# Kernel tuning notes

Measured on AMD Instinct MI355X. Metric: run time of the kernel, lower is better.

The kernel has to match this reference:

```python
import jax, jax.numpy as jnp
import numpy as np

K = 4
REG_MAX = 32


def setup_inputs() -> dict:
    key = jax.random.key(0)
    ks = jax.random.split(key, 6)
    B, L, C = 8, 100000, 80
    scores = jax.random.normal(ks[0], (B, L, C), dtype=jnp.float32)
    pred_corners = jax.random.normal(ks[1], (B, L, 4 * (REG_MAX + 1)), dtype=jnp.float32)
    in_dim = 4 * (K + 1)  # 20
    hidden = 64
    w1 = jax.random.normal(ks[2], (in_dim, hidden), dtype=jnp.float32) * (1.0 / np.sqrt(in_dim))
    b1 = jax.random.normal(ks[3], (hidden,), dtype=jnp.float32) * 0.01
    w2 = jax.random.normal(ks[4], (hidden, 1), dtype=jnp.float32) * (1.0 / np.sqrt(hidden))
    b2 = jax.random.normal(ks[5], (1,), dtype=jnp.float32) * 0.01
    return {"scores": scores, "pred_corners": pred_corners,
            "w1": w1, "b1": b1, "w2": w2, "b2": b2}


def reference(scores, pred_corners, w1, b1, w2, b2):
    B, L, _ = pred_corners.shape
    # [B, L, 4, reg_max+1]
    prob = jax.nn.softmax(pred_corners.reshape(B, L, 4, REG_MAX + 1), axis=-1)
    topk, _ = jax.lax.top_k(prob, K)                       # [B, L, 4, k]
    stat = jnp.concatenate([topk, topk.mean(-1, keepdims=True)], axis=-1)  # [B, L, 4, k+1]
    stat = stat.reshape(B, L, 4 * (K + 1))                 # [B, L, 20]
    h = jax.nn.silu(stat @ w1 + b1)                        # [B, L, 64]
    quality = h @ w2 + b2                                  # [B, L, 1]
    return scores + quality
```

## Files before the change

### kernel.cpp

```cpp
#include <hip/hip_runtime.h>

#define LOG2E 1.4426950408889634f

typedef __attribute__((address_space(3))) unsigned int lds_u32_t;
typedef const __attribute__((address_space(1))) unsigned int glb_u32_t;

__global__ __launch_bounds__(256) void lqe_wave(
    const float* __restrict__ scores,
    const float* __restrict__ pred,
    const float* __restrict__ w1,
    const float* __restrict__ b1,
    const float* __restrict__ w2,
    const float* __restrict__ b2,
    float* __restrict__ out)
{
    __shared__ __align__(16) float predS[4 * 2112];
    __shared__ __align__(16) float wS[1412];

    const int t    = threadIdx.x;
    const int lane = t & 63;
    const int wv   = t >> 6;
    const int tile = blockIdx.x;

#pragma unroll
    for (int k = 0; k < 5; ++k) wS[t + 256 * k] = w1[t + 256 * k];
    if (t < 64) { wS[1280 + t] = b1[t]; wS[1344 + t] = w2[t]; }
    if (t == 0) wS[1408] = b2[0];
    __syncthreads();

    const float* gp  = pred + (size_t)tile * 8448 + wv * 2112;
    float*       buf = predS + wv * 2112;
#pragma unroll
    for (int k = 0; k < 8; ++k) {
        __builtin_amdgcn_global_load_lds((glb_u32_t*)(gp + 256 * k + 4 * lane),
                                         (lds_u32_t*)(buf + 256 * k), 16, 0, 0);
    }
    __builtin_amdgcn_global_load_lds((glb_u32_t*)(gp + 2048 + lane),
                                     (lds_u32_t*)(buf + 2048), 4, 0, 0);

    asm volatile("s_waitcnt vmcnt(0)" ::: "memory");
    __builtin_amdgcn_sched_barrier(0);

    const size_t s4 = (size_t)tile * 1280 + wv * 320;
    const float4* sp = reinterpret_cast<const float4*>(scores) + s4;
    float4 sv0 = sp[lane +   0];
    float4 sv1 = sp[lane +  64];
    float4 sv2 = sp[lane + 128];
    float4 sv3 = sp[lane + 192];
    float4 sv4 = sp[lane + 256];

    const int r = lane >> 2, c = lane & 3;
    const float* xp = buf + r * 132 + c * 33;
    float xs[33];
#pragma unroll
    for (int j = 0; j < 33; ++j) xs[j] = xp[j];

    float t0 = -1e30f, t1 = -1e30f, t2 = -1e30f, t3 = -1e30f;
#pragma unroll
    for (int j = 0; j < 33; ++j) {
        float v  = xs[j];
        float r0 = fminf(t0, v);  t0 = fmaxf(t0, v);
        float r1 = fminf(t1, r0); t1 = fmaxf(t1, r0);
        float r2 = fminf(t2, r1); t2 = fmaxf(t2, r1);
        t3 = fmaxf(t3, r2);
    }
    float denom = 0.f;
#pragma unroll
    for (int j = 0; j < 33; ++j)
        denom += __builtin_amdgcn_exp2f((xs[j] - t0) * LOG2E);
    float rd = __builtin_amdgcn_rcpf(denom);

    float s5[5];
    s5[0] = rd;
    s5[1] = __builtin_amdgcn_exp2f((t1 - t0) * LOG2E) * rd;
    s5[2] = __builtin_amdgcn_exp2f((t2 - t0) * LOG2E) * rd;
    s5[3] = __builtin_amdgcn_exp2f((t3 - t0) * LOG2E) * rd;
    s5[4] = (s5[0] + s5[1] + s5[2] + s5[3]) * 0.25f;

    float stat[20];
#pragma unroll
    for (int i = 0; i < 20; ++i)
        stat[i] = __shfl(s5[i % 5], i / 5, 4);

    float hacc[16];
    {
        const float4* b1v = reinterpret_cast<const float4*>(wS + 1280 + 16 * c);
#pragma unroll
        for (int k = 0; k < 4; ++k) {
            float4 b = b1v[k];
            hacc[4*k+0]=b.x; hacc[4*k+1]=b.y; hacc[4*k+2]=b.z; hacc[4*k+3]=b.w;
        }
    }
#pragma unroll
    for (int i = 0; i < 20; ++i) {
        const float si = stat[i];
        const float4* wv4 = reinterpret_cast<const float4*>(wS + i * 64 + 16 * c);
#pragma unroll
        for (int k = 0; k < 4; ++k) {
            float4 w = wv4[k];
            hacc[4*k+0] = fmaf(si, w.x, hacc[4*k+0]);
            hacc[4*k+1] = fmaf(si, w.y, hacc[4*k+1]);
            hacc[4*k+2] = fmaf(si, w.z, hacc[4*k+2]);
            hacc[4*k+3] = fmaf(si, w.w, hacc[4*k+3]);
        }
    }
    float q = 0.f;
    {
        const float4* w2v = reinterpret_cast<const float4*>(wS + 1344 + 16 * c);
#pragma unroll
        for (int k = 0; k < 4; ++k) {
            float4 w = w2v[k];
#pragma unroll
            for (int e = 0; e < 4; ++e) {
                float v  = hacc[4*k+e];
                float sg = __builtin_amdgcn_rcpf(1.f + __builtin_amdgcn_exp2f(-v * LOG2E));
                float we = (e == 0) ? w.x : (e == 1) ? w.y : (e == 2) ? w.z : w.w;
                q = fmaf(v * sg, we, q);
            }
        }
    }
    q += __shfl_xor(q, 1, 4);
    q += __shfl_xor(q, 2, 4);
    q += wS[1408];

    float4* op = reinterpret_cast<float4*>(out) + s4;
    {
        float qq; int idx, rl;
        idx = lane +   0; rl = idx / 20; qq = __shfl(q, rl * 4, 64);
        sv0.x+=qq; sv0.y+=qq; sv0.z+=qq; sv0.w+=qq; op[idx] = sv0;
        idx = lane +  64; rl = idx / 20; qq = __shfl(q, rl * 4, 64);
        sv1.x+=qq; sv1.y+=qq; sv1.z+=qq; sv1.w+=qq; op[idx] = sv1;
        idx = lane + 128; rl = idx / 20; qq = __shfl(q, rl * 4, 64);
        sv2.x+=qq; sv2.y+=qq; sv2.z+=qq; sv2.w+=qq; op[idx] = sv2;
        idx = lane + 192; rl = idx / 20; qq = __shfl(q, rl * 4, 64);
        sv3.x+=qq; sv3.y+=qq; sv3.z+=qq; sv3.w+=qq; op[idx] = sv3;
        idx = lane + 256; rl = idx / 20; qq = __shfl(q, rl * 4, 64);
        sv4.x+=qq; sv4.y+=qq; sv4.z+=qq; sv4.w+=qq; op[idx] = sv4;
    }
}

extern "C" void kernel_launch(void* const* d_in, const int* in_sizes, int n_in,
                              void* d_out, int out_size, void* d_ws, size_t ws_size,
                              hipStream_t stream) {
    const float* scores = (const float*)d_in[0];
    const float* pred   = (const float*)d_in[1];
    const float* w1     = (const float*)d_in[2];
    const float* b1     = (const float*)d_in[3];
    const float* w2     = (const float*)d_in[4];
    const float* b2     = (const float*)d_in[5];
    float* out = (float*)d_out;

    const int nrows = in_sizes[1] / 132;
    const int grid  = nrows / 64;

    hipLaunchKernelGGL(lqe_wave, dim3(grid), dim3(256), 0, stream,
                       scores, pred, w1, b1, w2, b2, out);
}
```

Measured before the change: 172.5 us.

## Compute MLP hidden layer with fp16 MFMA and overlap weight staging with loads

Replaces the per-lane scalar FMA loop for the 20x64 first layer with one 16x16x32 f16 MFMA per 16-column block. Stat rows go through LDS and weights are packed to fp16. Weight staging now happens after the async global-to-LDS prefetch is issued, so the loads overlap it, and the second-layer reduction uses xor shuffles plus an LDS broadcast of q. This cuts VALU work and register pressure (launch bounds now request 4 blocks), but it adds fp16 rounding of the inputs and weights and extra LDS round trips.

```diff
diff --git a/kernel.cpp b/kernel.cpp
--- a/kernel.cpp
+++ b/kernel.cpp
@@ -4,8 +4,14 @@
 
 typedef __attribute__((address_space(3))) unsigned int lds_u32_t;
 typedef const __attribute__((address_space(1))) unsigned int glb_u32_t;
+typedef __fp16 h2v __attribute__((ext_vector_type(2)));
+typedef __fp16 v8h __attribute__((ext_vector_type(8)));
+typedef float  v4f __attribute__((ext_vector_type(4)));
 
-__global__ __launch_bounds__(256) void lqe_wave(
+union H2U { h2v h; unsigned int u; };
+union V8U { unsigned int u[4]; v8h v; };
+
+__global__ __launch_bounds__(256, 4) void lqe_mfma(
     const float* __restrict__ scores,
     const float* __restrict__ pred,
     const float* __restrict__ w1,
@@ -15,45 +21,50 @@
     float* __restrict__ out)
 {
     __shared__ __align__(16) float predS[4 * 2112];
-    __shared__ __align__(16) float wS[1412];
+    __shared__ __align__(16) unsigned int wHf[1024];
+    __shared__ __align__(16) float wSf[129];
+    __shared__ __align__(16) float qS[4][16];
 
-    const int t    = threadIdx.x;
-    const int lane = t & 63;
-    const int wv   = t >> 6;
+    const int t = threadIdx.x, lane = t & 63, wv = t >> 6;
     const int tile = blockIdx.x;
+    float* buf = predS + wv * 2112;
 
+    const float* gp = pred + (size_t)tile * 8448 + wv * 2112;
 #pragma unroll
-    for (int k = 0; k < 5; ++k) wS[t + 256 * k] = w1[t + 256 * k];
-    if (t < 64) { wS[1280 + t] = b1[t]; wS[1344 + t] = w2[t]; }
-    if (t == 0) wS[1408] = b2[0];
-    __syncthreads();
-
-    const float* gp  = pred + (size_t)tile * 8448 + wv * 2112;
-    float*       buf = predS + wv * 2112;
-#pragma unroll
-    for (int k = 0; k < 8; ++k) {
-        __builtin_amdgcn_global_load_lds((glb_u32_t*)(gp + 256 * k + 4 * lane),
-                                         (lds_u32_t*)(buf + 256 * k), 16, 0, 0);
-    }
+    for (int k = 0; k < 8; ++k)
+        __builtin_amdgcn_global_load_lds((glb_u32_t*)(gp + 256*k + 4*lane),
+                                         (lds_u32_t*)(buf + 256*k), 16, 0, 0);
     __builtin_amdgcn_global_load_lds((glb_u32_t*)(gp + 2048 + lane),
                                      (lds_u32_t*)(buf + 2048), 4, 0, 0);
 
-    asm volatile("s_waitcnt vmcnt(0)" ::: "memory");
-    __builtin_amdgcn_sched_barrier(0);
-
     const size_t s4 = (size_t)tile * 1280 + wv * 320;
     const float4* sp = reinterpret_cast<const float4*>(scores) + s4;
-    float4 sv0 = sp[lane +   0];
-    float4 sv1 = sp[lane +  64];
-    float4 sv2 = sp[lane + 128];
-    float4 sv3 = sp[lane + 192];
-    float4 sv4 = sp[lane + 256];
+    float4 sv0 = sp[lane], sv1 = sp[lane+64], sv2 = sp[lane+128],
+           sv3 = sp[lane+192], sv4 = sp[lane+256];
+
+#pragma unroll
+    for (int m = 0; m < 4; ++m) {
+        const int e  = t + 256*m;
+        const int bb = e >> 8, l = (e >> 2) & 63, d = e & 3;
+        const int n  = 16*bb + (l & 15);
+        const int k0 = 8*(l >> 4) + 2*d;
+        float a = 0.f, bfl = 0.f;
+        if (k0 < 20) { a = w1[k0*64 + n]; bfl = w1[k0*64 + 64 + n]; }
+        H2U hu; hu.h = __builtin_amdgcn_cvt_pkrtz(a, bfl);
+        wHf[e] = hu.u;
+    }
+    if (t < 64) { wSf[t] = b1[t]; wSf[64 + t] = w2[t]; }
+    if (t == 0) wSf[128] = b2[0];
+
+    __syncthreads();
 
     const int r = lane >> 2, c = lane & 3;
-    const float* xp = buf + r * 132 + c * 33;
+    const float* xp = buf + r*132 + c*33;
     float xs[33];
 #pragma unroll
     for (int j = 0; j < 33; ++j) xs[j] = xp[j];
+    asm volatile("s_waitcnt lgkmcnt(0)" ::: "memory");
+    __builtin_amdgcn_sched_barrier(0);
 
     float t0 = -1e30f, t1 = -1e30f, t2 = -1e30f, t3 = -1e30f;
 #pragma unroll
@@ -77,65 +88,71 @@
     s5[3] = __builtin_amdgcn_exp2f((t3 - t0) * LOG2E) * rd;
     s5[4] = (s5[0] + s5[1] + s5[2] + s5[3]) * 0.25f;
 
-    float stat[20];
+    float* st = buf;
 #pragma unroll
-    for (int i = 0; i < 20; ++i)
-        stat[i] = __shfl(s5[i % 5], i / 5, 4);
+    for (int i = 0; i < 5; ++i) st[r*36 + 5*c + i] = s5[i];
+#pragma unroll
+    for (int i = 0; i < 3; ++i) {
+        const int e = 3*lane + i;
+        st[(e/12)*36 + 20 + (e%12)] = 0.f;
+    }
+    asm volatile("s_waitcnt lgkmcnt(0)" ::: "memory");
+    __builtin_amdgcn_sched_barrier(0);
 
-    float hacc[16];
-    {
-        const float4* b1v = reinterpret_cast<const float4*>(wS + 1280 + 16 * c);
+    const int arow = lane & 15, aq = lane >> 4;
+    const float4* apv = reinterpret_cast<const float4*>(st + arow*36 + 8*aq);
+    float4 af0 = apv[0], af1 = apv[1];
+    V8U ua;
+    { H2U h0; h0.h = __builtin_amdgcn_cvt_pkrtz(af0.x, af0.y); ua.u[0] = h0.u; }
+    { H2U h1; h1.h = __builtin_amdgcn_cvt_pkrtz(af0.z, af0.w); ua.u[1] = h1.u; }
+    { H2U h2; h2.h = __builtin_amdgcn_cvt_pkrtz(af1.x, af1.y); ua.u[2] = h2.u; }
+    { H2U h3; h3.h = __builtin_amdgcn_cvt_pkrtz(af1.z, af1.w); ua.u[3] = h3.u; }
+    const v8h afrag = ua.v;
+
+    const uint4* wfv = reinterpret_cast<const uint4*>(wHf);
+    v4f acc[4];
 #pragma unroll
-        for (int k = 0; k < 4; ++k) {
-            float4 b = b1v[k];
-            hacc[4*k+0]=b.x; hacc[4*k+1]=b.y; hacc[4*k+2]=b.z; hacc[4*k+3]=b.w;
-        }
+    for (int bb = 0; bb < 4; ++bb) {
+        uint4 bw = wfv[bb*64 + lane];
+        V8U ub; ub.u[0]=bw.x; ub.u[1]=bw.y; ub.u[2]=bw.z; ub.u[3]=bw.w;
+        const float bias = wSf[16*bb + arow];
+        v4f cc = { bias, bias, bias, bias };
+        acc[bb] = __builtin_amdgcn_mfma_f32_16x16x32_f16(afrag, ub.v, cc, 0, 0, 0);
+    }
+
+    float qp0 = 0.f, qp1 = 0.f, qp2 = 0.f, qp3 = 0.f;
+#pragma unroll
+    for (int bb = 0; bb < 4; ++bb) {
+        const float w2l = wSf[64 + 16*bb + arow];
+        float v, sg;
+        v = acc[bb][0]; sg = __builtin_amdgcn_rcpf(1.f + __builtin_amdgcn_exp2f(-v*LOG2E)); qp0 = fmaf(v*sg, w2l, qp0);
+        v = acc[bb][1]; sg = __builtin_amdgcn_rcpf(1.f + __builtin_amdgcn_exp2f(-v*LOG2E)); qp1 = fmaf(v*sg, w2l, qp1);
+        v = acc[bb][2]; sg = __builtin_amdgcn_rcpf(1.f + __builtin_amdgcn_exp2f(-v*LOG2E)); qp2 = fmaf(v*sg, w2l, qp2);
+        v = acc[bb][3]; sg = __builtin_amdgcn_rcpf(1.f + __builtin_amdgcn_exp2f(-v*LOG2E)); qp3 = fmaf(v*sg, w2l, qp3);
     }
 #pragma unroll
-    for (int i = 0; i < 20; ++i) {
-        const float si = stat[i];
-        const float4* wv4 = reinterpret_cast<const float4*>(wS + i * 64 + 16 * c);
-#pragma unroll
-        for (int k = 0; k < 4; ++k) {
-            float4 w = wv4[k];
-            hacc[4*k+0] = fmaf(si, w.x, hacc[4*k+0]);
-            hacc[4*k+1] = fmaf(si, w.y, hacc[4*k+1]);
-            hacc[4*k+2] = fmaf(si, w.z, hacc[4*k+2]);
-            hacc[4*k+3] = fmaf(si, w.w, hacc[4*k+3]);
-        }
+    for (int m = 1; m < 16; m <<= 1) {
+        qp0 += __shfl_xor(qp0, m, 64);
+        qp1 += __shfl_xor(qp1, m, 64);
+        qp2 += __shfl_xor(qp2, m, 64);
+        qp3 += __shfl_xor(qp3, m, 64);
     }
-    float q = 0.f;
-    {
-        const float4* w2v = reinterpret_cast<const float4*>(wS + 1344 + 16 * c);
-#pragma unroll
-        for (int k = 0; k < 4; ++k) {
-            float4 w = w2v[k];
-#pragma unroll
-            for (int e = 0; e < 4; ++e) {
-                float v  = hacc[4*k+e];
-                float sg = __builtin_amdgcn_rcpf(1.f + __builtin_amdgcn_exp2f(-v * LOG2E));
-                float we = (e == 0) ? w.x : (e == 1) ? w.y : (e == 2) ? w.z : w.w;
-                q = fmaf(v * sg, we, q);
-            }
-        }
+    if (arow == 0) {
+        const float bq = wSf[128];
+        float4 qv = { qp0 + bq, qp1 + bq, qp2 + bq, qp3 + bq };
+        *reinterpret_cast<float4*>(&qS[wv][4*aq]) = qv;
     }
-    q += __shfl_xor(q, 1, 4);
-    q += __shfl_xor(q, 2, 4);
-    q += wS[1408];
+    asm volatile("s_waitcnt lgkmcnt(0)" ::: "memory");
+    __builtin_amdgcn_sched_barrier(0);
 
     float4* op = reinterpret_cast<float4*>(out) + s4;
     {
-        float qq; int idx, rl;
-        idx = lane +   0; rl = idx / 20; qq = __shfl(q, rl * 4, 64);
-        sv0.x+=qq; sv0.y+=qq; sv0.z+=qq; sv0.w+=qq; op[idx] = sv0;
-        idx = lane +  64; rl = idx / 20; qq = __shfl(q, rl * 4, 64);
-        sv1.x+=qq; sv1.y+=qq; sv1.z+=qq; sv1.w+=qq; op[idx] = sv1;
-        idx = lane + 128; rl = idx / 20; qq = __shfl(q, rl * 4, 64);
-        sv2.x+=qq; sv2.y+=qq; sv2.z+=qq; sv2.w+=qq; op[idx] = sv2;
-        idx = lane + 192; rl = idx / 20; qq = __shfl(q, rl * 4, 64);
-        sv3.x+=qq; sv3.y+=qq; sv3.z+=qq; sv3.w+=qq; op[idx] = sv3;
-        idx = lane + 256; rl = idx / 20; qq = __shfl(q, rl * 4, 64);
-        sv4.x+=qq; sv4.y+=qq; sv4.z+=qq; sv4.w+=qq; op[idx] = sv4;
+        float qq; int idx;
+        idx = lane;       qq = qS[wv][idx/20]; sv0.x+=qq; sv0.y+=qq; sv0.z+=qq; sv0.w+=qq; op[idx] = sv0;
+        idx = lane +  64; qq = qS[wv][idx/20]; sv1.x+=qq; sv1.y+=qq; sv1.z+=qq; sv1.w+=qq; op[idx] = sv1;
+        idx = lane + 128; qq = qS[wv][idx/20]; sv2.x+=qq; sv2.y+=qq; sv2.z+=qq; sv2.w+=qq; op[idx] = sv2;
+        idx = lane + 192; qq = qS[wv][idx/20]; sv3.x+=qq; sv3.y+=qq; sv3.z+=qq; sv3.w+=qq; op[idx] = sv3;
+        idx = lane + 256; qq = qS[wv][idx/20]; sv4.x+=qq; sv4.y+=qq; sv4.z+=qq; sv4.w+=qq; op[idx] = sv4;
     }
 }
 
@@ -153,6 +170,6 @@
     const int nrows = in_sizes[1] / 132;
     const int grid  = nrows / 64;
 
-    hipLaunchKernelGGL(lqe_wave, dim3(grid), dim3(256), 0, stream,
+    hipLaunchKernelGGL(lqe_mfma, dim3(grid), dim3(256), 0, stream,
                        scores, pred, w1, b1, w2, b2, out);
 }
```

Result: slower. 191.6 us (+11.1%).
